# Kernel tuning notes

Measured on AMD Instinct MI355X. Metric: run time of the kernel, lower is better.

## Reference

```python
import jax, jax.numpy as jnp
import numpy as np

B, S, D, H = 4, 2048, 1024, 16
HD = D // H  # head_dim = 64


def setup_inputs() -> dict:
    key = jax.random.key(0)
    ks = jax.random.split(key, 10)
    sc = 0.02
    return {
        "data": jax.random.normal(ks[0], (B, S, D), jnp.float32),
        "context": jax.random.normal(ks[1], (B, S, D), jnp.float32),
        "Wq": jax.random.normal(ks[2], (D, D), jnp.float32) * sc,
        "bq": jnp.zeros((D,), jnp.float32),
        "Wk": jax.random.normal(ks[3], (D, D), jnp.float32) * sc,
        "bk": jnp.zeros((D,), jnp.float32),
        "Wv": jax.random.normal(ks[4], (D, D), jnp.float32) * sc,
        "bv": jnp.zeros((D,), jnp.float32),
        "Wo": jax.random.normal(ks[5], (D, D), jnp.float32) * sc,
        "bo": jnp.zeros((D,), jnp.float32),
    }


def reference(data, context, Wq, bq, Wk, bk, Wv, bv, Wo, bo):
    # Q/K/V projections (nn.Linear: x @ W^T + b; here weights stored as [in, out])
    Q = data @ Wq + bq            # [B,S,D]
    K = context @ Wk + bk
    V = context @ Wv + bv
    # split heads -> [B,H,S,HD]
    Q = Q.reshape(B, S, H, HD).transpose(0, 2, 1, 3)
    K = K.reshape(B, S, H, HD).transpose(0, 2, 1, 3)
    V = V.reshape(B, S, H, HD).transpose(0, 2, 1, 3)
    scale = jnp.sqrt(jnp.asarray(HD, Q.dtype))
    Z = jnp.einsum("bhqd,bhkd->bhqk", Q, K) / scale   # [B,H,S,S]
    # causal mask: row >= col allowed
    row = jnp.arange(S)[:, None]
    col = jnp.arange(S)[None, :]
    Z = jnp.where(row >= col, Z, jnp.asarray(-jnp.inf, Z.dtype))
    Z = jax.nn.softmax(Z, axis=-1)
    out = jnp.einsum("bhqk,bhkd->bhqd", Z, V)         # [B,H,S,HD]
    out = out.transpose(0, 2, 1, 3).reshape(B, S, D)
    return out @ Wo + bo
```

## Files before the change

kernel.cpp:

```cpp
#include <hip/hip_runtime.h>
#include <hip/hip_bf16.h>

#define B_ 4
#define S_ 2048
#define D_ 1024
#define H_ 16
#define HD_ 64
#define M_ (B_*S_)

typedef __bf16 bf16;
typedef __bf16 bf16v4 __attribute__((ext_vector_type(4)));
typedef __bf16 bf16v8 __attribute__((ext_vector_type(8)));
typedef float f32x4 __attribute__((ext_vector_type(4)));
typedef float f32x16 __attribute__((ext_vector_type(16)));

#define GLDS(gp, lp) __builtin_amdgcn_global_load_lds( \
    (const __attribute__((address_space(1))) void*)(gp), \
    (__attribute__((address_space(3))) void*)(lp), 16, 0, 0)

__global__ void cast2_bf16_kernel(const float* __restrict__ a, const float* __restrict__ b,
                                  bf16* __restrict__ oa, bf16* __restrict__ ob, int n) {
    int gid = blockIdx.x * blockDim.x + threadIdx.x;
    int i = gid * 8;
    const float* src; bf16* dst;
    if (i < n) { src = a + i; dst = oa + i; }
    else       { src = b + (i - n); dst = ob + (i - n); }
    const float4* p = reinterpret_cast<const float4*>(src);
    float4 x = p[0], y = p[1];
    bf16v8 o;
    o[0] = (bf16)x.x; o[1] = (bf16)x.y; o[2] = (bf16)x.z; o[3] = (bf16)x.w;
    o[4] = (bf16)y.x; o[5] = (bf16)y.y; o[6] = (bf16)y.z; o[7] = (bf16)y.w;
    *reinterpret_cast<bf16v8*>(dst) = o;
}

__global__ void transpose4_kernel(const float* __restrict__ W0, const float* __restrict__ W1,
                                  const float* __restrict__ W2, const float* __restrict__ W3,
                                  bf16* __restrict__ T0, bf16* __restrict__ T1,
                                  bf16* __restrict__ T2, bf16* __restrict__ T3,
                                  float s0) {
    __shared__ float tile[32][33];
    int which = blockIdx.z;
    const float* W = which == 0 ? W0 : which == 1 ? W1 : which == 2 ? W2 : W3;
    bf16* Wt       = which == 0 ? T0 : which == 1 ? T1 : which == 2 ? T2 : T3;
    float scale    = which == 0 ? s0 : 1.f;
    int kb = blockIdx.y * 32, nb = blockIdx.x * 32;
    int t = threadIdx.x;
    int c = t & 31, r0 = t >> 5;
    for (int i = 0; i < 4; ++i) {
        int r = r0 + i * 8;
        tile[r][c] = W[(size_t)(kb + r) * D_ + nb + c];
    }
    __syncthreads();
    for (int i = 0; i < 4; ++i) {
        int r = r0 + i * 8;
        Wt[(size_t)(nb + r) * D_ + kb + c] = (bf16)(tile[c][r] * scale);
    }
}

template<int MODE>
__global__ __launch_bounds__(256) void gemm128_kernel(const bf16* __restrict__ A,
                                                      const bf16* __restrict__ Bt,
                                                      const float* __restrict__ bias,
                                                      float bias_scale,
                                                      void* __restrict__ Cout,
                                                      int M, int N, int K) {
    __shared__ bf16 Asm[128 * 64];
    __shared__ bf16 Bsm[128 * 64];
    int mb = blockIdx.x * 128, nb = blockIdx.y * 128;
    int t = threadIdx.x, l = t & 63, w = t >> 6;
    int wr = w >> 1, wc = w & 1;
    int lg = l >> 4, lr = l & 15;
    f32x4 acc[4][4] = {};
    int srow = t >> 3;
    int schk = t & 7;
    for (int k0 = 0; k0 < K; k0 += 64) {
        __syncthreads();
        #pragma unroll
        for (int p = 0; p < 4; ++p) {
            int row = p * 32 + srow;
            int ca = schk ^ (row & 7);
            GLDS(&A[(size_t)(mb + row) * K + k0 + ca * 8], &Asm[(size_t)(p * 256 + t) * 8]);
            GLDS(&Bt[(size_t)(nb + row) * K + k0 + ca * 8], &Bsm[(size_t)(p * 256 + t) * 8]);
        }
        __syncthreads();
        #pragma unroll
        for (int kk = 0; kk < 2; ++kk) {
            bf16v8 af[4], bfv[4];
            #pragma unroll
            for (int i = 0; i < 4; ++i) {
                int ra = wr * 64 + i * 16 + lr;
                af[i]  = *(const bf16v8*)&Asm[ra * 64 + (((kk * 4 + lg) ^ (ra & 7)) * 8)];
                int rb = wc * 64 + i * 16 + lr;
                bfv[i] = *(const bf16v8*)&Bsm[rb * 64 + (((kk * 4 + lg) ^ (rb & 7)) * 8)];
            }
            #pragma unroll
            for (int i = 0; i < 4; ++i)
                #pragma unroll
                for (int j = 0; j < 4; ++j)
                    acc[i][j] = __builtin_amdgcn_mfma_f32_16x16x32_bf16(af[i], bfv[j], acc[i][j], 0, 0, 0);
        }
    }
    #pragma unroll
    for (int i = 0; i < 4; ++i)
        #pragma unroll
        for (int j = 0; j < 4; ++j) {
            int col = nb + wc * 64 + j * 16 + lr;
            float bv = bias ? bias[col] * bias_scale : 0.f;
            int row0 = mb + wr * 64 + i * 16 + lg * 4;
            if (MODE == 2) {
                int b = row0 >> 11, s = row0 & 2047;
                int bh = b * 16 + (col >> 6), hd = col & 63;
                bf16v4 ov;
                #pragma unroll
                for (int r = 0; r < 4; ++r) ov[r] = (bf16)(acc[i][j][r] + bv);
                *(bf16v4*)&((bf16*)Cout)[((size_t)bh * 64 + hd) * 2048 + s] = ov;
            } else {
                #pragma unroll
                for (int r = 0; r < 4; ++r) {
                    int row = row0 + r;
                    float v = acc[i][j][r] + bv;
                    if (MODE == 1) ((float*)Cout)[(size_t)row * N + col] = v;
                    else           ((bf16*)Cout)[(size_t)row * N + col] = (bf16)v;
                }
            }
        }
}

__global__ __launch_bounds__(256, 2) void attn_kernel(const bf16* __restrict__ Q,
                                                      const bf16* __restrict__ Kb,
                                                      const bf16* __restrict__ Vt,
                                                      bf16* __restrict__ O) {
    __shared__ bf16 Ksm[2][64 * 64];
    __shared__ bf16 Vsm[2][64 * 64];

    int id = (int)blockIdx.x;
    int bh = id & 63;
    int qi = (S_ / 128 - 1) - (id >> 6);
    int qb = qi * 128;
    int b = bh >> 4, h = bh & 15;
    int t = threadIdx.x, w = t >> 6, l = t & 63;
    int ln = l & 31, hi = l >> 5;
    int qwave = qb + w * 32;
    int q = qwave + ln;

    const bf16* kbase = Kb + (size_t)(b * S_) * D_ + h * HD_;
    const bf16* vbase = Vt + (size_t)bh * HD_ * S_;
    const bf16* qptr  = Q + (size_t)(b * S_ + q) * D_ + h * HD_;

    bf16v8 qf[4];
    #pragma unroll
    for (int c = 0; c < 4; ++c)
        qf[c] = *(const bf16v8*)(qptr + c * 16 + hi * 8);

    bf16v8 ones;
    #pragma unroll
    for (int e = 0; e < 8; ++e) ones[e] = (bf16)1.0f;

    f32x16 o0 = {}, o1 = {};
    f32x16 ls = {};

    int srow = t >> 3, schk = t & 7;
    int nT = 2 * qi + 2;

    auto stage = [&](int kv0, int bufsel) {
        #pragma unroll
        for (int p = 0; p < 2; ++p) {
            int row = p * 32 + srow;
            int cs = schk ^ (row & 7);
            GLDS(kbase + (size_t)(kv0 + row) * D_ + cs * 8, &Ksm[bufsel][p * 2048 + t * 8]);
            GLDS(vbase + (size_t)row * S_ + kv0 + cs * 8,   &Vsm[bufsel][p * 2048 + t * 8]);
        }
    };

    stage(0, 0);
    for (int tt = 0; tt < nT; ++tt) {
        int cur = tt & 1;
        int kv0 = tt * 64;
        __syncthreads();
        if (tt + 1 < nT) stage(kv0 + 64, cur ^ 1);
        if (kv0 > qwave + 31) continue;

        f32x16 st0 = {}, st1 = {};
        __builtin_amdgcn_s_setprio(1);
        #pragma unroll
        for (int c = 0; c < 4; ++c) {
            int r0 = ln;
            bf16v8 kf0 = *(const bf16v8*)&Ksm[cur][r0 * 64 + (((2 * c + hi) ^ (r0 & 7)) * 8)];
            st0 = __builtin_amdgcn_mfma_f32_32x32x16_bf16(kf0, qf[c], st0, 0, 0, 0);
            int r1 = 32 + ln;
            bf16v8 kf1 = *(const bf16v8*)&Ksm[cur][r1 * 64 + (((2 * c + hi) ^ (r1 & 7)) * 8)];
            st1 = __builtin_amdgcn_mfma_f32_32x32x16_bf16(kf1, qf[c], st1, 0, 0, 0);
        }
        __builtin_amdgcn_s_setprio(0);

        if (kv0 + 63 > qwave) {
            #pragma unroll
            for (int rg = 0; rg < 16; ++rg) {
                int kvo = (rg & 3) + 8 * (rg >> 2) + 4 * hi;
                if (kv0 + kvo > q)      st0[rg] = -__builtin_inff();
                if (kv0 + 32 + kvo > q) st1[rg] = -__builtin_inff();
            }
        }

        #pragma unroll
        for (int i = 0; i < 16; ++i) {
            st0[i] = __builtin_exp2f(st0[i]);
            st1[i] = __builtin_exp2f(st1[i]);
        }

        uint32_t x0[4][2], x1[4][2];
        #pragma unroll
        for (int j = 0; j < 4; ++j) {
            asm("v_cvt_pk_bf16_f32 %0, %1, %2" : "=v"(x0[j][0]) : "v"(st0[4*j+0]), "v"(st0[4*j+1]));
            asm("v_cvt_pk_bf16_f32 %0, %1, %2" : "=v"(x0[j][1]) : "v"(st0[4*j+2]), "v"(st0[4*j+3]));
            asm("v_cvt_pk_bf16_f32 %0, %1, %2" : "=v"(x1[j][0]) : "v"(st1[4*j+0]), "v"(st1[4*j+1]));
            asm("v_cvt_pk_bf16_f32 %0, %1, %2" : "=v"(x1[j][1]) : "v"(st1[4*j+2]), "v"(st1[4*j+3]));
        }
        union PB { uint32_t u[4]; bf16v8 v; };
        PB pb[4];
        #pragma unroll
        for (int c = 0; c < 4; ++c) {
            uint32_t (*xs)[2] = (c >> 1) ? x1 : x0;
            int cp = c & 1;
            #pragma unroll
            for (int d = 0; d < 2; ++d) {
                uint32_t own_lo = xs[2 * cp][d];
                uint32_t own_hi = xs[2 * cp + 1][d];
                uint32_t par_lo = __shfl_xor(own_lo, 32, 64);
                uint32_t par_hi = __shfl_xor(own_hi, 32, 64);
                pb[c].u[d]     = hi ? par_hi : own_lo;
                pb[c].u[2 + d] = hi ? own_hi : par_lo;
            }
        }

        __builtin_amdgcn_s_setprio(1);
        #pragma unroll
        for (int c = 0; c < 4; ++c) {
            int r0 = ln;
            bf16v8 va0 = *(const bf16v8*)&Vsm[cur][r0 * 64 + (((2 * c + hi) ^ (r0 & 7)) * 8)];
            o0 = __builtin_amdgcn_mfma_f32_32x32x16_bf16(va0, pb[c].v, o0, 0, 0, 0);
            int r1 = 32 + ln;
            bf16v8 va1 = *(const bf16v8*)&Vsm[cur][r1 * 64 + (((2 * c + hi) ^ (r1 & 7)) * 8)];
            o1 = __builtin_amdgcn_mfma_f32_32x32x16_bf16(va1, pb[c].v, o1, 0, 0, 0);
            ls = __builtin_amdgcn_mfma_f32_32x32x16_bf16(ones, pb[c].v, ls, 0, 0, 0);
        }
        __builtin_amdgcn_s_setprio(0);
    }

    float li = 1.f / ls[0];
    bf16* obase = O + (size_t)(b * S_ + q) * D_ + h * HD_;
    #pragma unroll
    for (int j = 0; j < 4; ++j) {
        bf16v4 ov;
        #pragma unroll
        for (int r = 0; r < 4; ++r) ov[r] = (bf16)(o0[4 * j + r] * li);
        *(bf16v4*)(obase + 8 * j + 4 * hi) = ov;
    }
    #pragma unroll
    for (int j = 0; j < 4; ++j) {
        bf16v4 ov;
        #pragma unroll
        for (int r = 0; r < 4; ++r) ov[r] = (bf16)(o1[4 * j + r] * li);
        *(bf16v4*)(obase + 32 + 8 * j + 4 * hi) = ov;
    }
}

extern "C" void kernel_launch(void* const* d_in, const int* in_sizes, int n_in,
                              void* d_out, int out_size, void* d_ws, size_t ws_size,
                              hipStream_t stream) {
    const float* data    = (const float*)d_in[0];
    const float* context = (const float*)d_in[1];
    const float* Wq = (const float*)d_in[2];
    const float* bq = (const float*)d_in[3];
    const float* Wk = (const float*)d_in[4];
    const float* bk = (const float*)d_in[5];
    const float* Wv = (const float*)d_in[6];
    const float* bv = (const float*)d_in[7];
    const float* Wo = (const float*)d_in[8];
    const float* bo = (const float*)d_in[9];
    float* out = (float*)d_out;

    char* ws = (char*)d_ws;
    size_t off = 0;
    auto alloc = [&](size_t bytes) { void* p = ws + off; off += (bytes + 255) & ~255ull; return p; };
    bf16* dataB = (bf16*)alloc((size_t)M_ * D_ * 2);
    bf16* ctxB  = (bf16*)alloc((size_t)M_ * D_ * 2);
    bf16* WqT   = (bf16*)alloc((size_t)D_ * D_ * 2);
    bf16* WkT   = (bf16*)alloc((size_t)D_ * D_ * 2);
    bf16* WvT   = (bf16*)alloc((size_t)D_ * D_ * 2);
    bf16* WoT   = (bf16*)alloc((size_t)D_ * D_ * 2);
    bf16* Qb    = (bf16*)alloc((size_t)M_ * D_ * 2);
    bf16* Kb    = (bf16*)alloc((size_t)M_ * D_ * 2);
    bf16* Vt    = (bf16*)alloc((size_t)M_ * D_ * 2);
    bf16* Ob    = ctxB;

    const float qscale = 0.125f * 1.44269504088896340736f;

    int nTok = M_ * D_;
    cast2_bf16_kernel<<<2 * nTok / 2048, 256, 0, stream>>>(data, context, dataB, ctxB, nTok);

    dim3 tg(D_ / 32, D_ / 32, 4);
    transpose4_kernel<<<tg, 256, 0, stream>>>(Wq, Wk, Wv, Wo, WqT, WkT, WvT, WoT, qscale);

    dim3 gg(M_ / 128, D_ / 128);
    gemm128_kernel<0><<<gg, 256, 0, stream>>>(dataB, WqT, bq, qscale, Qb, M_, D_, D_);
    gemm128_kernel<0><<<gg, 256, 0, stream>>>(ctxB,  WkT, bk, 1.f,    Kb, M_, D_, D_);
    gemm128_kernel<2><<<gg, 256, 0, stream>>>(ctxB,  WvT, bv, 1.f,    Vt, M_, D_, D_);

    attn_kernel<<<dim3(S_ / 128 * B_ * H_), 256, 0, stream>>>(Qb, Kb, Vt, Ob);

    gemm128_kernel<1><<<gg, 256, 0, stream>>>(Ob, WoT, bo, 1.f, out, M_, D_, D_);
}
```

Measured before the change: 187.4 us.

## Merge prep kernels, batch QKV GEMMs, use double-buffered 256x128 GEMM tiles

Fuses the bf16 cast and the weight transpose into a single prep launch. The three QKV projection GEMMs now run as one launch with z selecting the operands, and the output projection reuses the same kernel. The GEMM grows to 256x128 tiles with 512 threads and double-buffers its LDS stages so global loads for the next K-slice overlap the MFMA work on the current one. This cuts launch count and tail effects and improves latency hiding, at the cost of more LDS per block (96KB), which may limit occupancy.

```diff
diff --git a/kernel.cpp b/kernel.cpp
--- a/kernel.cpp
+++ b/kernel.cpp
@@ -7,6 +7,7 @@
 #define H_ 16
 #define HD_ 64
 #define M_ (B_*S_)
+#define NTOK (M_*D_)
 
 typedef __bf16 bf16;
 typedef __bf16 bf16v4 __attribute__((ext_vector_type(4)));
@@ -18,80 +19,101 @@
     (const __attribute__((address_space(1))) void*)(gp), \
     (__attribute__((address_space(3))) void*)(lp), 16, 0, 0)
 
-__global__ void cast2_bf16_kernel(const float* __restrict__ a, const float* __restrict__ b,
-                                  bf16* __restrict__ oa, bf16* __restrict__ ob, int n) {
-    int gid = blockIdx.x * blockDim.x + threadIdx.x;
-    int i = gid * 8;
-    const float* src; bf16* dst;
-    if (i < n) { src = a + i; dst = oa + i; }
-    else       { src = b + (i - n); dst = ob + (i - n); }
-    const float4* p = reinterpret_cast<const float4*>(src);
-    float4 x = p[0], y = p[1];
-    bf16v8 o;
-    o[0] = (bf16)x.x; o[1] = (bf16)x.y; o[2] = (bf16)x.z; o[3] = (bf16)x.w;
-    o[4] = (bf16)y.x; o[5] = (bf16)y.y; o[6] = (bf16)y.z; o[7] = (bf16)y.w;
-    *reinterpret_cast<bf16v8*>(dst) = o;
+__global__ void prep_kernel(const float* __restrict__ data, const float* __restrict__ ctx,
+                            bf16* __restrict__ dataB, bf16* __restrict__ ctxB,
+                            const float* __restrict__ W0, const float* __restrict__ W1,
+                            const float* __restrict__ W2, const float* __restrict__ W3,
+                            bf16* __restrict__ T0, bf16* __restrict__ T1,
+                            bf16* __restrict__ T2, bf16* __restrict__ T3,
+                            float s0) {
+    int bid = blockIdx.x;
+    if (bid < 8192) {
+        int i = (bid * 256 + (int)threadIdx.x) * 8;
+        const float* src; bf16* dst;
+        if (i < NTOK) { src = data + i; dst = dataB + i; }
+        else          { src = ctx + (i - NTOK); dst = ctxB + (i - NTOK); }
+        const float4* p = reinterpret_cast<const float4*>(src);
+        float4 x = p[0], y = p[1];
+        bf16v8 o;
+        o[0] = (bf16)x.x; o[1] = (bf16)x.y; o[2] = (bf16)x.z; o[3] = (bf16)x.w;
+        o[4] = (bf16)y.x; o[5] = (bf16)y.y; o[6] = (bf16)y.z; o[7] = (bf16)y.w;
+        *reinterpret_cast<bf16v8*>(dst) = o;
+    } else {
+        __shared__ float tile[32][33];
+        int local = bid - 8192;
+        int which = local >> 10;
+        int rem = local & 1023;
+        const float* W = which == 0 ? W0 : which == 1 ? W1 : which == 2 ? W2 : W3;
+        bf16* Wt       = which == 0 ? T0 : which == 1 ? T1 : which == 2 ? T2 : T3;
+        float scale    = which == 0 ? s0 : 1.f;
+        int nb = (rem & 31) * 32, kb = (rem >> 5) * 32;
+        int t = threadIdx.x;
+        int c = t & 31, r0 = t >> 5;
+        for (int i = 0; i < 4; ++i) {
+            int r = r0 + i * 8;
+            tile[r][c] = W[(size_t)(kb + r) * D_ + nb + c];
+        }
+        __syncthreads();
+        for (int i = 0; i < 4; ++i) {
+            int r = r0 + i * 8;
+            Wt[(size_t)(nb + r) * D_ + kb + c] = (bf16)(tile[c][r] * scale);
+        }
+    }
 }
 
-__global__ void transpose4_kernel(const float* __restrict__ W0, const float* __restrict__ W1,
-                                  const float* __restrict__ W2, const float* __restrict__ W3,
-                                  bf16* __restrict__ T0, bf16* __restrict__ T1,
-                                  bf16* __restrict__ T2, bf16* __restrict__ T3,
-                                  float s0) {
-    __shared__ float tile[32][33];
-    int which = blockIdx.z;
-    const float* W = which == 0 ? W0 : which == 1 ? W1 : which == 2 ? W2 : W3;
-    bf16* Wt       = which == 0 ? T0 : which == 1 ? T1 : which == 2 ? T2 : T3;
-    float scale    = which == 0 ? s0 : 1.f;
-    int kb = blockIdx.y * 32, nb = blockIdx.x * 32;
-    int t = threadIdx.x;
-    int c = t & 31, r0 = t >> 5;
-    for (int i = 0; i < 4; ++i) {
-        int r = r0 + i * 8;
-        tile[r][c] = W[(size_t)(kb + r) * D_ + nb + c];
-    }
-    __syncthreads();
-    for (int i = 0; i < 4; ++i) {
-        int r = r0 + i * 8;
-        Wt[(size_t)(nb + r) * D_ + kb + c] = (bf16)(tile[c][r] * scale);
-    }
-}
-
-template<int MODE>
-__global__ __launch_bounds__(256) void gemm128_kernel(const bf16* __restrict__ A,
-                                                      const bf16* __restrict__ Bt,
-                                                      const float* __restrict__ bias,
-                                                      float bias_scale,
-                                                      void* __restrict__ Cout,
-                                                      int M, int N, int K) {
-    __shared__ bf16 Asm[128 * 64];
-    __shared__ bf16 Bsm[128 * 64];
-    int mb = blockIdx.x * 128, nb = blockIdx.y * 128;
+__global__ __launch_bounds__(512, 2) void gemm_big_kernel(
+        const bf16* __restrict__ dataB, const bf16* __restrict__ ctxB, const bf16* __restrict__ Ob,
+        const bf16* __restrict__ WqT, const bf16* __restrict__ WkT,
+        const bf16* __restrict__ WvT, const bf16* __restrict__ WoT,
+        const float* __restrict__ bq, const float* __restrict__ bk,
+        const float* __restrict__ bv, const float* __restrict__ bo,
+        bf16* __restrict__ Qb, bf16* __restrict__ Kb, bf16* __restrict__ Vt,
+        float* __restrict__ outp, float qscale, int zofs) {
+    __shared__ bf16 Asm[2][256 * 64];
+    __shared__ bf16 Bsm[2][128 * 64];
+    int z = blockIdx.z + zofs;
+    const bf16* A; const bf16* Bt; const float* bias; float bscale = 1.f;
+    if (z == 0)      { A = dataB; Bt = WqT; bias = bq; bscale = qscale; }
+    else if (z == 1) { A = ctxB;  Bt = WkT; bias = bk; }
+    else if (z == 2) { A = ctxB;  Bt = WvT; bias = bv; }
+    else             { A = Ob;    Bt = WoT; bias = bo; }
+
+    int mb = blockIdx.x * 256, nb = blockIdx.y * 128;
     int t = threadIdx.x, l = t & 63, w = t >> 6;
     int wr = w >> 1, wc = w & 1;
     int lg = l >> 4, lr = l & 15;
     f32x4 acc[4][4] = {};
-    int srow = t >> 3;
-    int schk = t & 7;
-    for (int k0 = 0; k0 < K; k0 += 64) {
-        __syncthreads();
+    int srow = t >> 3, schk = t & 7;
+
+    auto stage = [&](int k0, int buf) {
         #pragma unroll
         for (int p = 0; p < 4; ++p) {
-            int row = p * 32 + srow;
-            int ca = schk ^ (row & 7);
-            GLDS(&A[(size_t)(mb + row) * K + k0 + ca * 8], &Asm[(size_t)(p * 256 + t) * 8]);
-            GLDS(&Bt[(size_t)(nb + row) * K + k0 + ca * 8], &Bsm[(size_t)(p * 256 + t) * 8]);
-        }
-        __syncthreads();
+            int row = p * 64 + srow;
+            int cs = schk ^ (row & 7);
+            GLDS(&A[(size_t)(mb + row) * D_ + k0 + cs * 8], &Asm[buf][(size_t)(p * 512 + t) * 8]);
+        }
+        #pragma unroll
+        for (int p = 0; p < 2; ++p) {
+            int row = p * 64 + srow;
+            int cs = schk ^ (row & 7);
+            GLDS(&Bt[(size_t)(nb + row) * D_ + k0 + cs * 8], &Bsm[buf][(size_t)(p * 512 + t) * 8]);
+        }
+    };
+
+    stage(0, 0);
+    __syncthreads();
+    for (int tt = 0; tt < 16; ++tt) {
+        int cur = tt & 1;
+        if (tt < 15) stage((tt + 1) * 64, cur ^ 1);
         #pragma unroll
         for (int kk = 0; kk < 2; ++kk) {
             bf16v8 af[4], bfv[4];
             #pragma unroll
             for (int i = 0; i < 4; ++i) {
                 int ra = wr * 64 + i * 16 + lr;
-                af[i]  = *(const bf16v8*)&Asm[ra * 64 + (((kk * 4 + lg) ^ (ra & 7)) * 8)];
+                af[i]  = *(const bf16v8*)&Asm[cur][ra * 64 + (((kk * 4 + lg) ^ (ra & 7)) * 8)];
                 int rb = wc * 64 + i * 16 + lr;
-                bfv[i] = *(const bf16v8*)&Bsm[rb * 64 + (((kk * 4 + lg) ^ (rb & 7)) * 8)];
+                bfv[i] = *(const bf16v8*)&Bsm[cur][rb * 64 + (((kk * 4 + lg) ^ (rb & 7)) * 8)];
             }
             #pragma unroll
             for (int i = 0; i < 4; ++i)
@@ -99,29 +121,32 @@
                 for (int j = 0; j < 4; ++j)
                     acc[i][j] = __builtin_amdgcn_mfma_f32_16x16x32_bf16(af[i], bfv[j], acc[i][j], 0, 0, 0);
         }
-    }
+        __syncthreads();
+    }
+
     #pragma unroll
     for (int i = 0; i < 4; ++i)
         #pragma unroll
         for (int j = 0; j < 4; ++j) {
             int col = nb + wc * 64 + j * 16 + lr;
-            float bv = bias ? bias[col] * bias_scale : 0.f;
+            float bvv = bias[col] * bscale;
             int row0 = mb + wr * 64 + i * 16 + lg * 4;
-            if (MODE == 2) {
+            if (z == 2) {
                 int b = row0 >> 11, s = row0 & 2047;
                 int bh = b * 16 + (col >> 6), hd = col & 63;
                 bf16v4 ov;
                 #pragma unroll
-                for (int r = 0; r < 4; ++r) ov[r] = (bf16)(acc[i][j][r] + bv);
-                *(bf16v4*)&((bf16*)Cout)[((size_t)bh * 64 + hd) * 2048 + s] = ov;
+                for (int r = 0; r < 4; ++r) ov[r] = (bf16)(acc[i][j][r] + bvv);
+                *(bf16v4*)&Vt[((size_t)bh * 64 + hd) * 2048 + s] = ov;
+            } else if (z == 3) {
+                #pragma unroll
+                for (int r = 0; r < 4; ++r)
+                    outp[(size_t)(row0 + r) * D_ + col] = acc[i][j][r] + bvv;
             } else {
+                bf16* dst = (z == 0) ? Qb : Kb;
                 #pragma unroll
-                for (int r = 0; r < 4; ++r) {
-                    int row = row0 + r;
-                    float v = acc[i][j][r] + bv;
-                    if (MODE == 1) ((float*)Cout)[(size_t)row * N + col] = v;
-                    else           ((bf16*)Cout)[(size_t)row * N + col] = (bf16)v;
-                }
+                for (int r = 0; r < 4; ++r)
+                    dst[(size_t)(row0 + r) * D_ + col] = (bf16)(acc[i][j][r] + bvv);
             }
         }
 }
@@ -296,18 +321,14 @@
 
     const float qscale = 0.125f * 1.44269504088896340736f;
 
-    int nTok = M_ * D_;
-    cast2_bf16_kernel<<<2 * nTok / 2048, 256, 0, stream>>>(data, context, dataB, ctxB, nTok);
-
-    dim3 tg(D_ / 32, D_ / 32, 4);
-    transpose4_kernel<<<tg, 256, 0, stream>>>(Wq, Wk, Wv, Wo, WqT, WkT, WvT, WoT, qscale);
-
-    dim3 gg(M_ / 128, D_ / 128);
-    gemm128_kernel<0><<<gg, 256, 0, stream>>>(dataB, WqT, bq, qscale, Qb, M_, D_, D_);
-    gemm128_kernel<0><<<gg, 256, 0, stream>>>(ctxB,  WkT, bk, 1.f,    Kb, M_, D_, D_);
-    gemm128_kernel<2><<<gg, 256, 0, stream>>>(ctxB,  WvT, bv, 1.f,    Vt, M_, D_, D_);
+    prep_kernel<<<12288, 256, 0, stream>>>(data, context, dataB, ctxB,
+                                           Wq, Wk, Wv, Wo, WqT, WkT, WvT, WoT, qscale);
+
+    gemm_big_kernel<<<dim3(M_ / 256, D_ / 128, 3), 512, 0, stream>>>(
+        dataB, ctxB, Ob, WqT, WkT, WvT, WoT, bq, bk, bv, bo, Qb, Kb, Vt, out, qscale, 0);
 
     attn_kernel<<<dim3(S_ / 128 * B_ * H_), 256, 0, stream>>>(Qb, Kb, Vt, Ob);
 
-    gemm128_kernel<1><<<gg, 256, 0, stream>>>(Ob, WoT, bo, 1.f, out, M_, D_, D_);
+    gemm_big_kernel<<<dim3(M_ / 256, D_ / 128, 1), 512, 0, stream>>>(
+        dataB, ctxB, Ob, WqT, WkT, WvT, WoT, bq, bk, bv, bo, Qb, Kb, Vt, out, qscale, 3);
 }
```

Measured after the change: 191.7 us. +2.3%, slower.
